# Optimization experiments

Measured on AMD Instinct MI355X. Metric: run time of the kernel, lower is better.

Reference implementation:

```python
import jax, jax.numpy as jnp
import numpy as np

NEG_SLOPE = 0.01  # torch LeakyReLU default

def leaky_relu(x):
    return jnp.where(x >= 0, x, NEG_SLOPE * x)

def setup_inputs() -> dict:
    key = jax.random.key(0)
    ks = jax.random.split(key, 12)
    D = 128
    N_U, N_I, E = 100000, 50000, 1000000
    s = 1.0 / np.sqrt(D)
    return {
        "h_user": jax.random.normal(ks[0], (N_U, D), jnp.float32),
        "h_item": jax.random.normal(ks[1], (N_I, D), jnp.float32),
        "src_idx": jax.random.randint(ks[2], (E,), 0, N_U, jnp.int64) if jax.config.jax_enable_x64 else jax.random.randint(ks[2], (E,), 0, N_U, jnp.int32),
        "dst_idx": jax.random.randint(ks[3], (E,), 0, N_I, jnp.int32),
        "W_left": jax.random.normal(ks[4], (D, D), jnp.float32) * s,
        "b_left": jax.random.normal(ks[5], (D,), jnp.float32) * s,
        "W_right": jax.random.normal(ks[6], (D, D), jnp.float32) * s,
        "b_right": jax.random.normal(ks[7], (D,), jnp.float32) * s,
        "W1": jax.random.normal(ks[8], (D, D), jnp.float32) * s,
        "b1": jax.random.normal(ks[9], (D,), jnp.float32) * s,
        "W2": jax.random.normal(ks[10], (D, 1), jnp.float32) * s,
        "b2": jax.random.normal(ks[11], (1,), jnp.float32) * s,
    }

def reference(h_user, h_item, src_idx, dst_idx,
              W_left, b_left, W_right, b_right, W1, b1, W2, b2):
    # node linear transforms (dropout is identity in eval mode)
    u_f = h_user @ W_left + b_left      # [N_u, D]
    i_f = h_item @ W_right + b_right    # [N_i, D]
    # edge gather + add (dgl fn.u_add_v)
    score = u_f[src_idx] + i_f[dst_idx]  # [E, D]
    # pred MLP: LeakyReLU -> Linear(D,D) -> LeakyReLU -> Linear(D,1) -> LeakyReLU
    x = leaky_relu(score)
    x = leaky_relu(x @ W1 + b1)
    x = leaky_relu(x @ W2 + b2)         # [E, 1]
    return x
```

## Files before the change

### kernel.cpp

```cpp
#include <hip/hip_runtime.h>

typedef __attribute__((ext_vector_type(8))) short bf16x8;
typedef __attribute__((ext_vector_type(4))) float f32x4;
typedef __attribute__((ext_vector_type(2))) float f32x2;

__device__ __forceinline__ float leaky(float v) { return fmaxf(v, 0.01f * v); }

__device__ __forceinline__ unsigned short f2bf(float a) {
    unsigned int u = __float_as_uint(a);
    return (unsigned short)((u + 0x7FFFu + ((u >> 16) & 1u)) >> 16);
}

__device__ __forceinline__ unsigned int cvtpk(float a, float b) {
#if __has_builtin(__builtin_amdgcn_cvt_pk_bf16_f32)
    typedef __attribute__((ext_vector_type(2))) __bf16 bf2_t;
    bf2_t v = __builtin_amdgcn_cvt_pk_bf16_f32(a, b);
    return __builtin_bit_cast(unsigned int, v);
#else
    unsigned int ua = __float_as_uint(a);
    ua = (ua + 0x7FFFu + ((ua >> 16) & 1u)) >> 16;
    unsigned int ub = __float_as_uint(b);
    ub = (ub + 0x7FFFu + ((ub >> 16) & 1u)) >> 16;
    return ua | (ub << 16);
#endif
}

__device__ __forceinline__ f32x2 unpk2(unsigned int d) {
    f32x2 r;
    r.x = __uint_as_float(d << 16);
    r.y = __uint_as_float(d & 0xFFFF0000u);
    return r;
}

__device__ __forceinline__ unsigned int mix1(unsigned int u, unsigned int i) {
    f32x2 v = unpk2(u) + unpk2(i);
    v = __builtin_elementwise_max(v, v * 0.01f);
    return cvtpk(v.x, v.y);
}

__global__ __launch_bounds__(128) void prep(const float* __restrict__ WL,
                                            const float* __restrict__ WR,
                                            const float* __restrict__ W1,
                                            unsigned short* __restrict__ WLf,
                                            unsigned short* __restrict__ WRf,
                                            unsigned short* __restrict__ Wf) {
    int g = blockIdx.x;
    int f = (g & 127) * 128 + threadIdx.x;
    int j = f & 7, lane = (f >> 3) & 63, nt = (f >> 9) & 7, kb = f >> 12;
    int n = nt * 16 + (lane & 15);
    int kf = kb * 32 + (lane >> 4) * 8 + j;
    if (g < 128) {
        WLf[f] = f2bf(WL[kf * 128 + n]);
    } else if (g < 256) {
        WRf[f] = f2bf(WR[kf * 128 + n]);
    } else {
        int k = (kf & 7) * 16 + (kf >> 3);
        Wf[f] = f2bf(W1[k * 128 + n]);
    }
}

#define PITCH 136

__global__ __launch_bounds__(512, 8) void node_mfma2(const float* __restrict__ h_user,
                                                     const float* __restrict__ h_item,
                                                     const unsigned short* __restrict__ WLf,
                                                     const unsigned short* __restrict__ WRf,
                                                     const float* __restrict__ b_left,
                                                     const float* __restrict__ b_right,
                                                     unsigned short* __restrict__ u_f,
                                                     unsigned short* __restrict__ i_f,
                                                     int N_U, int N_I, int BU) {
    bool isU = (int)blockIdx.x < BU;
    const float* h = isU ? h_user : h_item;
    const unsigned short* Wfr = isU ? WLf : WRf;
    const float* b = isU ? b_left : b_right;
    unsigned short* out = isU ? u_f : i_f;
    int N = isU ? N_U : N_I;
    int r0 = (isU ? blockIdx.x : blockIdx.x - BU) * 128;

    __shared__ unsigned short xt[128 * PITCH];
    int t = threadIdx.x;
    int s = t & 31;
    int el0 = t >> 5;

    f32x4 g[8];
#pragma unroll
    for (int pass = 0; pass < 8; ++pass) {
        int row = min(r0 + pass * 16 + el0, N - 1);
        g[pass] = *(const f32x4*)(h + (size_t)row * 128 + s * 4);
    }
#pragma unroll
    for (int pass = 0; pass < 8; ++pass) {
        int el = pass * 16 + el0;
        unsigned int* rp = (unsigned int*)(xt + el * PITCH + s * 4);
        rp[0] = cvtpk(g[pass].x, g[pass].y);
        rp[1] = cvtpk(g[pass].z, g[pass].w);
    }
    __syncthreads();

    int wave = t >> 6;
    int lane = t & 63;
    int col = lane & 15;
    int quad = lane >> 4;
    int wp = wave >> 1;
    int ch = wave & 1;
    int m0 = wp * 32;

    f32x4 acc[2][4];
#pragma unroll
    for (int mt = 0; mt < 2; ++mt)
#pragma unroll
        for (int i = 0; i < 4; ++i) acc[mt][i] = (f32x4){0.f, 0.f, 0.f, 0.f};

#pragma unroll
    for (int kb = 0; kb < 4; ++kb) {
        bf16x8 afr[2];
#pragma unroll
        for (int mt = 0; mt < 2; ++mt)
            afr[mt] = *(const bf16x8*)(xt + (m0 + mt * 16 + col) * PITCH + kb * 32 + quad * 8);
#pragma unroll
        for (int i = 0; i < 4; ++i) {
            int nt = ch * 4 + i;
            bf16x8 bfr = *(const bf16x8*)(Wfr + ((kb * 8 + nt) * 64 + lane) * 8);
            acc[0][i] = __builtin_amdgcn_mfma_f32_16x16x32_bf16(afr[0], bfr, acc[0][i], 0, 0, 0);
            acc[1][i] = __builtin_amdgcn_mfma_f32_16x16x32_bf16(afr[1], bfr, acc[1][i], 0, 0, 0);
        }
    }

    float bb[4];
#pragma unroll
    for (int i = 0; i < 4; ++i) bb[i] = b[(ch * 4 + i) * 16 + col];
#pragma unroll
    for (int mt = 0; mt < 2; ++mt)
#pragma unroll
        for (int rr = 0; rr < 4; ++rr) {
            int row = r0 + m0 + mt * 16 + quad * 4 + rr;
            uint2 v;
            v.x = cvtpk(acc[mt][0][rr] + bb[0], acc[mt][1][rr] + bb[1]);
            v.y = cvtpk(acc[mt][2][rr] + bb[2], acc[mt][3][rr] + bb[3]);
            if (row < N) *(uint2*)(out + (size_t)row * 128 + col * 8 + ch * 4) = v;
        }
}

#define TE 128

__global__ __launch_bounds__(512, 6) void edge_kernel(
    const unsigned short* __restrict__ u_f, const unsigned short* __restrict__ i_f,
    const int* __restrict__ src, const int* __restrict__ dst,
    const unsigned short* __restrict__ Wf,
    const float* __restrict__ b1, const float* __restrict__ W2,
    const float* __restrict__ b2, float* __restrict__ out, int E) {
    __shared__ unsigned short xt[TE * PITCH];
    __shared__ float zb[4][2][32];
    int t = threadIdx.x;
    int e0 = blockIdx.x * TE;

    int s = t & 15;
    int el0 = t >> 4;

    int su[4], sd[4];
#pragma unroll
    for (int pass = 0; pass < 4; ++pass) {
        int ec = min(e0 + pass * 32 + el0, E - 1);
        su[pass] = src[ec];
        sd[pass] = dst[ec];
    }
    uint4 ug[4], ig[4];
#pragma unroll
    for (int pass = 0; pass < 4; ++pass) {
        ug[pass] = *(const uint4*)(u_f + (size_t)su[pass] * 128 + s * 8);
        ig[pass] = *(const uint4*)(i_f + (size_t)sd[pass] * 128 + s * 8);
    }
#pragma unroll
    for (int pass = 0; pass < 4; ++pass) {
        uint4 a;
        a.x = mix1(ug[pass].x, ig[pass].x);
        a.y = mix1(ug[pass].y, ig[pass].y);
        a.z = mix1(ug[pass].z, ig[pass].z);
        a.w = mix1(ug[pass].w, ig[pass].w);
        *(uint4*)(xt + (pass * 32 + el0) * PITCH + s * 8) = a;
    }
    __syncthreads();

    int wave = t >> 6;
    int lane = t & 63;
    int col = lane & 15;
    int quad = lane >> 4;
    int wp = wave >> 1;
    int ch = wave & 1;
    int m0 = wp * 32;

    f32x4 acc[2][4];
#pragma unroll
    for (int mt = 0; mt < 2; ++mt)
#pragma unroll
        for (int i = 0; i < 4; ++i) acc[mt][i] = (f32x4){0.f, 0.f, 0.f, 0.f};

#pragma unroll
    for (int kb = 0; kb < 4; ++kb) {
        bf16x8 afr[2];
#pragma unroll
        for (int mt = 0; mt < 2; ++mt)
            afr[mt] = *(const bf16x8*)(xt + (m0 + mt * 16 + col) * PITCH + kb * 32 + quad * 8);
#pragma unroll
        for (int i = 0; i < 4; ++i) {
            int nt = ch * 4 + i;
            bf16x8 bfr = *(const bf16x8*)(Wf + ((kb * 8 + nt) * 64 + lane) * 8);
            acc[0][i] = __builtin_amdgcn_mfma_f32_16x16x32_bf16(afr[0], bfr, acc[0][i], 0, 0, 0);
            acc[1][i] = __builtin_amdgcn_mfma_f32_16x16x32_bf16(afr[1], bfr, acc[1][i], 0, 0, 0);
        }
    }

    f32x4 p[2];
#pragma unroll
    for (int mt = 0; mt < 2; ++mt) p[mt] = (f32x4){0.f, 0.f, 0.f, 0.f};

#pragma unroll
    for (int i = 0; i < 4; ++i) {
        int n = (ch * 4 + i) * 16 + col;
        float bb = b1[n];
        float ww = W2[n];
#pragma unroll
        for (int mt = 0; mt < 2; ++mt) {
            f32x4 y = acc[mt][i] + bb;
            y = __builtin_elementwise_max(y, y * 0.01f);
            p[mt] += y * ww;
        }
    }
#pragma unroll
    for (int off = 1; off < 16; off <<= 1)
#pragma unroll
        for (int mt = 0; mt < 2; ++mt)
#pragma unroll
            for (int rr = 0; rr < 4; ++rr) p[mt][rr] += __shfl_xor(p[mt][rr], off, 64);

    if (col == 0) {
#pragma unroll
        for (int mt = 0; mt < 2; ++mt)
#pragma unroll
            for (int rr = 0; rr < 4; ++rr)
                zb[wp][ch][mt * 16 + quad * 4 + rr] = p[mt][rr];
    }
    __syncthreads();

    if (t < 128) {
        int g = t >> 5;
        int idx = t & 31;
        float z = zb[g][0][idx] + zb[g][1][idx] + b2[0];
        int e = e0 + g * 32 + idx;
        if (e < E) out[e] = leaky(z);
    }
}

extern "C" void kernel_launch(void* const* d_in, const int* in_sizes, int n_in,
                              void* d_out, int out_size, void* d_ws, size_t ws_size,
                              hipStream_t stream) {
    const float* h_user  = (const float*)d_in[0];
    const float* h_item  = (const float*)d_in[1];
    const int*   src_idx = (const int*)d_in[2];
    const int*   dst_idx = (const int*)d_in[3];
    const float* W_left  = (const float*)d_in[4];
    const float* b_left  = (const float*)d_in[5];
    const float* W_right = (const float*)d_in[6];
    const float* b_right = (const float*)d_in[7];
    const float* W1      = (const float*)d_in[8];
    const float* b1      = (const float*)d_in[9];
    const float* W2      = (const float*)d_in[10];
    const float* b2      = (const float*)d_in[11];
    float* out = (float*)d_out;

    int N_U = in_sizes[0] / 128;
    int N_I = in_sizes[1] / 128;
    int E   = in_sizes[2];

    unsigned short* Wf  = (unsigned short*)d_ws;
    unsigned short* WLf = Wf + 16384;
    unsigned short* WRf = WLf + 16384;
    unsigned short* u_f = (unsigned short*)((char*)d_ws + 131072);
    unsigned short* i_f = u_f + (size_t)N_U * 128;

    prep<<<384, 128, 0, stream>>>(W_left, W_right, W1, WLf, WRf, Wf);

    int BU = (N_U + 127) / 128;
    int BI = (N_I + 127) / 128;
    node_mfma2<<<BU + BI, 512, 0, stream>>>(h_user, h_item, WLf, WRf, b_left, b_right,
                                            u_f, i_f, N_U, N_I, BU);

    edge_kernel<<<(E + TE - 1) / TE, 512, 0, stream>>>(u_f, i_f, src_idx, dst_idx,
                                                       Wf, b1, W2, b2, out, E);
}
```

Baseline: 226.4 us.

## Make edge kernel persistent over four tiles with prefetched gathers and LDS-staged W1

Each edge block now handles four 128-edge tiles instead of one. It copies the bf16 W1 fragments into LDS once per block and software-pipelines the next tile's index loads and row gathers behind the current tile's MFMA and reduction work. This is meant to hide gather latency and cut the repeated global W1 fragment loads and per-block setup. The cost is more LDS per block (an extra 32KB), a lower occupancy bound (4 blocks instead of 6 for this kernel, and 6 instead of 8 for the node kernel), and fewer blocks in the grid.

```diff
diff --git a/kernel.cpp b/kernel.cpp
--- a/kernel.cpp
+++ b/kernel.cpp
@@ -61,7 +61,7 @@
 
 #define PITCH 136
 
-__global__ __launch_bounds__(512, 8) void node_mfma2(const float* __restrict__ h_user,
+__global__ __launch_bounds__(512, 6) void node_mfma2(const float* __restrict__ h_user,
                                                      const float* __restrict__ h_item,
                                                      const unsigned short* __restrict__ WLf,
                                                      const unsigned short* __restrict__ WRf,
@@ -143,44 +143,20 @@
 }
 
 #define TE 128
-
-__global__ __launch_bounds__(512, 6) void edge_kernel(
+#define NT 4
+
+__global__ __launch_bounds__(512, 4) void edge_kernel(
     const unsigned short* __restrict__ u_f, const unsigned short* __restrict__ i_f,
     const int* __restrict__ src, const int* __restrict__ dst,
     const unsigned short* __restrict__ Wf,
     const float* __restrict__ b1, const float* __restrict__ W2,
     const float* __restrict__ b2, float* __restrict__ out, int E) {
-    __shared__ unsigned short xt[TE * PITCH];
+    __shared__ __attribute__((aligned(16))) unsigned short xt[TE * PITCH];
+    __shared__ __attribute__((aligned(16))) unsigned short wl[16384];
     __shared__ float zb[4][2][32];
     int t = threadIdx.x;
-    int e0 = blockIdx.x * TE;
-
     int s = t & 15;
     int el0 = t >> 4;
-
-    int su[4], sd[4];
-#pragma unroll
-    for (int pass = 0; pass < 4; ++pass) {
-        int ec = min(e0 + pass * 32 + el0, E - 1);
-        su[pass] = src[ec];
-        sd[pass] = dst[ec];
-    }
-    uint4 ug[4], ig[4];
-#pragma unroll
-    for (int pass = 0; pass < 4; ++pass) {
-        ug[pass] = *(const uint4*)(u_f + (size_t)su[pass] * 128 + s * 8);
-        ig[pass] = *(const uint4*)(i_f + (size_t)sd[pass] * 128 + s * 8);
-    }
-#pragma unroll
-    for (int pass = 0; pass < 4; ++pass) {
-        uint4 a;
-        a.x = mix1(ug[pass].x, ig[pass].x);
-        a.y = mix1(ug[pass].y, ig[pass].y);
-        a.z = mix1(ug[pass].z, ig[pass].z);
-        a.w = mix1(ug[pass].w, ig[pass].w);
-        *(uint4*)(xt + (pass * 32 + el0) * PITCH + s * 8) = a;
-    }
-    __syncthreads();
 
     int wave = t >> 6;
     int lane = t & 63;
@@ -190,65 +166,138 @@
     int ch = wave & 1;
     int m0 = wp * 32;
 
-    f32x4 acc[2][4];
-#pragma unroll
-    for (int mt = 0; mt < 2; ++mt)
-#pragma unroll
-        for (int i = 0; i < 4; ++i) acc[mt][i] = (f32x4){0.f, 0.f, 0.f, 0.f};
-
-#pragma unroll
-    for (int kb = 0; kb < 4; ++kb) {
-        bf16x8 afr[2];
-#pragma unroll
-        for (int mt = 0; mt < 2; ++mt)
-            afr[mt] = *(const bf16x8*)(xt + (m0 + mt * 16 + col) * PITCH + kb * 32 + quad * 8);
-#pragma unroll
-        for (int i = 0; i < 4; ++i) {
-            int nt = ch * 4 + i;
-            bf16x8 bfr = *(const bf16x8*)(Wf + ((kb * 8 + nt) * 64 + lane) * 8);
-            acc[0][i] = __builtin_amdgcn_mfma_f32_16x16x32_bf16(afr[0], bfr, acc[0][i], 0, 0, 0);
-            acc[1][i] = __builtin_amdgcn_mfma_f32_16x16x32_bf16(afr[1], bfr, acc[1][i], 0, 0, 0);
-        }
-    }
-
-    f32x4 p[2];
-#pragma unroll
-    for (int mt = 0; mt < 2; ++mt) p[mt] = (f32x4){0.f, 0.f, 0.f, 0.f};
-
+    float bb[4], ww[4];
 #pragma unroll
     for (int i = 0; i < 4; ++i) {
         int n = (ch * 4 + i) * 16 + col;
-        float bb = b1[n];
-        float ww = W2[n];
-#pragma unroll
-        for (int mt = 0; mt < 2; ++mt) {
-            f32x4 y = acc[mt][i] + bb;
-            y = __builtin_elementwise_max(y, y * 0.01f);
-            p[mt] += y * ww;
-        }
-    }
-#pragma unroll
-    for (int off = 1; off < 16; off <<= 1)
+        bb[i] = b1[n];
+        ww[i] = W2[n];
+    }
+    float b2v = b2[0];
+
+#pragma unroll
+    for (int i = 0; i < 4; ++i)
+        ((uint4*)wl)[i * 512 + t] = ((const uint4*)Wf)[i * 512 + t];
+
+    int e00 = blockIdx.x * (NT * TE);
+    int su[4], sd[4];
+    uint4 ug[4], ig[4];
+
+#pragma unroll
+    for (int p = 0; p < 4; ++p) {
+        int ec = min(e00 + p * 32 + el0, E - 1);
+        su[p] = src[ec];
+        sd[p] = dst[ec];
+    }
+#pragma unroll
+    for (int p = 0; p < 4; ++p) {
+        ug[p] = *(const uint4*)(u_f + (size_t)su[p] * 128 + s * 8);
+        ig[p] = *(const uint4*)(i_f + (size_t)sd[p] * 128 + s * 8);
+    }
+#pragma unroll
+    for (int p = 0; p < 4; ++p) {
+        uint4 a;
+        a.x = mix1(ug[p].x, ig[p].x);
+        a.y = mix1(ug[p].y, ig[p].y);
+        a.z = mix1(ug[p].z, ig[p].z);
+        a.w = mix1(ug[p].w, ig[p].w);
+        *(uint4*)(xt + (p * 32 + el0) * PITCH + s * 8) = a;
+    }
+    __syncthreads();
+
+    for (int k = 0; k < NT; ++k) {
+        int e0 = e00 + k * TE;
+        bool pf = (k + 1 < NT);
+
+        if (pf) {
+#pragma unroll
+            for (int p = 0; p < 4; ++p) {
+                int ec = min(e0 + TE + p * 32 + el0, E - 1);
+                su[p] = src[ec];
+                sd[p] = dst[ec];
+            }
+            __builtin_amdgcn_sched_barrier(0);
+        }
+
+        f32x4 acc[2][4];
 #pragma unroll
         for (int mt = 0; mt < 2; ++mt)
 #pragma unroll
-            for (int rr = 0; rr < 4; ++rr) p[mt][rr] += __shfl_xor(p[mt][rr], off, 64);
-
-    if (col == 0) {
-#pragma unroll
-        for (int mt = 0; mt < 2; ++mt)
-#pragma unroll
-            for (int rr = 0; rr < 4; ++rr)
-                zb[wp][ch][mt * 16 + quad * 4 + rr] = p[mt][rr];
-    }
-    __syncthreads();
-
-    if (t < 128) {
-        int g = t >> 5;
-        int idx = t & 31;
-        float z = zb[g][0][idx] + zb[g][1][idx] + b2[0];
-        int e = e0 + g * 32 + idx;
-        if (e < E) out[e] = leaky(z);
+            for (int i = 0; i < 4; ++i) acc[mt][i] = (f32x4){0.f, 0.f, 0.f, 0.f};
+
+#pragma unroll
+        for (int kb = 0; kb < 4; ++kb) {
+            bf16x8 afr[2];
+#pragma unroll
+            for (int mt = 0; mt < 2; ++mt)
+                afr[mt] = *(const bf16x8*)(xt + (m0 + mt * 16 + col) * PITCH + kb * 32 + quad * 8);
+#pragma unroll
+            for (int i = 0; i < 4; ++i) {
+                int nt = ch * 4 + i;
+                bf16x8 bfr = *(const bf16x8*)(wl + ((kb * 8 + nt) * 64 + lane) * 8);
+                acc[0][i] = __builtin_amdgcn_mfma_f32_16x16x32_bf16(afr[0], bfr, acc[0][i], 0, 0, 0);
+                acc[1][i] = __builtin_amdgcn_mfma_f32_16x16x32_bf16(afr[1], bfr, acc[1][i], 0, 0, 0);
+            }
+        }
+
+        if (pf) {
+#pragma unroll
+            for (int p = 0; p < 4; ++p) {
+                ug[p] = *(const uint4*)(u_f + (size_t)su[p] * 128 + s * 8);
+                ig[p] = *(const uint4*)(i_f + (size_t)sd[p] * 128 + s * 8);
+            }
+            __builtin_amdgcn_sched_barrier(0);
+        }
+
+        f32x4 pz[2];
+#pragma unroll
+        for (int mt = 0; mt < 2; ++mt) pz[mt] = (f32x4){0.f, 0.f, 0.f, 0.f};
+
+#pragma unroll
+        for (int i = 0; i < 4; ++i) {
+#pragma unroll
+            for (int mt = 0; mt < 2; ++mt) {
+                f32x4 y = acc[mt][i] + bb[i];
+                y = __builtin_elementwise_max(y, y * 0.01f);
+                pz[mt] += y * ww[i];
+            }
+        }
+#pragma unroll
+        for (int off = 1; off < 16; off <<= 1)
+#pragma unroll
+            for (int mt = 0; mt < 2; ++mt)
+#pragma unroll
+                for (int rr = 0; rr < 4; ++rr) pz[mt][rr] += __shfl_xor(pz[mt][rr], off, 64);
+
+        if (col == 0) {
+#pragma unroll
+            for (int mt = 0; mt < 2; ++mt)
+#pragma unroll
+                for (int rr = 0; rr < 4; ++rr)
+                    zb[wp][ch][mt * 16 + quad * 4 + rr] = pz[mt][rr];
+        }
+        __syncthreads();
+
+        if (t < 128) {
+            int g = t >> 5;
+            int idx = t & 31;
+            float z = zb[g][0][idx] + zb[g][1][idx] + b2v;
+            int e = e0 + g * 32 + idx;
+            if (e < E) out[e] = leaky(z);
+        }
+
+        if (pf) {
+#pragma unroll
+            for (int p = 0; p < 4; ++p) {
+                uint4 a;
+                a.x = mix1(ug[p].x, ig[p].x);
+                a.y = mix1(ug[p].y, ig[p].y);
+                a.z = mix1(ug[p].z, ig[p].z);
+                a.w = mix1(ug[p].w, ig[p].w);
+                *(uint4*)(xt + (p * 32 + el0) * PITCH + s * 8) = a;
+            }
+        }
+        __syncthreads();
     }
 }
 
@@ -286,6 +335,8 @@
     node_mfma2<<<BU + BI, 512, 0, stream>>>(h_user, h_item, WLf, WRf, b_left, b_right,
                                             u_f, i_f, N_U, N_I, BU);
 
-    edge_kernel<<<(E + TE - 1) / TE, 512, 0, stream>>>(u_f, i_f, src_idx, dst_idx,
-                                                       Wf, b1, W2, b2, out, E);
-}
+    int TILES = (E + TE - 1) / TE;
+    int NB = (TILES + NT - 1) / NT;
+    edge_kernel<<<NB, 512, 0, stream>>>(u_f, i_f, src_idx, dst_idx,
+                                        Wf, b1, W2, b2, out, E);
+}
```

New measurement: 251.6 us. +11.1%, slower.
